# Kernel optimization log

Measured on AMD Instinct MI355X. Metric: run time of the kernel, lower is better.

The kernel has to match this reference:

```python
import jax, jax.numpy as jnp
import numpy as np

B, C, W, H = 16, 256, 32, 32
HEADS = 4


def setup_inputs() -> dict:
    key = jax.random.key(0)
    ks = jax.random.split(key, 9)
    d = C // HEADS
    return {
        "x": jax.random.normal(ks[0], (B, C, W, H), jnp.float32),
        "Wq": jax.random.normal(ks[1], (C, C), jnp.float32) * 0.05,
        "bq": jax.random.normal(ks[2], (C,), jnp.float32) * 0.05,
        "Wk": jax.random.normal(ks[3], (C, C), jnp.float32) * 0.05,
        "bk": jax.random.normal(ks[4], (C,), jnp.float32) * 0.05,
        "Wv": jax.random.normal(ks[5], (C, C), jnp.float32) * 0.05,
        "bv": jax.random.normal(ks[6], (C,), jnp.float32) * 0.05,
        "rel_h": jax.random.normal(ks[7], (1, HEADS, d, 1, H), jnp.float32),
        "rel_w": jax.random.normal(ks[8], (1, HEADS, d, W, 1), jnp.float32),
    }


def reference(x, Wq, bq, Wk, bk, Wv, bv, rel_h, rel_w):
    b, c, w, h = x.shape
    heads = rel_h.shape[1]
    d = c // heads
    n = w * h  # sequence length = spatial positions
    xf = x.reshape(b, c, n)

    def proj(Wt, bt):
        # 1x1 conv == per-position linear over channels
        y = jnp.einsum('oc,bcn->bon', Wt, xf) + bt[None, :, None]
        return y.reshape(b, heads, d, n)

    q = proj(Wq, bq)
    k = proj(Wk, bk)
    v = proj(Wv, bv)

    # similarity = q^T k : [b, heads, n, n]
    sim = jnp.einsum('bhdi,bhdj->bhij', q, k)
    # relative position bias content term: rel^T q
    rel = (rel_h + rel_w).reshape(heads, d, n)  # broadcast-add then flatten spatial
    qpos = jnp.einsum('hdi,bhdj->bhij', rel, q)

    attn = jax.nn.softmax(sim + qpos, axis=-1)
    # out = v @ attn^T : [b, heads, d, n]
    out = jnp.einsum('bhdn,bhmn->bhdm', v, attn)
    return out.reshape(b, c, w, h)
```

## Files before the change

kernel.cpp:

```cpp
#include <hip/hip_runtime.h>

constexpr int Bb  = 16;
constexpr int Cch = 256;
constexpr int NH  = 4;
constexpr int Dh  = 64;
constexpr int Nn  = 1024;

typedef _Float16 f16;
typedef __attribute__((ext_vector_type(8))) _Float16 f16x8;
typedef __attribute__((ext_vector_type(4))) _Float16 f16x4;
typedef __attribute__((ext_vector_type(4))) float    f32x4;

#define LOG2E 1.44269504088896f

__device__ inline void gld16(const f16* g, const f16* lds_wave_base) {
    __builtin_amdgcn_global_load_lds(
        (const __attribute__((address_space(1))) unsigned int*)g,
        (__attribute__((address_space(3))) unsigned int*)lds_wave_base,
        16, 0, 0);
}

__global__ __launch_bounds__(256) void prep_kernel(
    const float* __restrict__ x,
    const float* __restrict__ Wq, const float* __restrict__ Wk,
    const float* __restrict__ Wv,
    const float* __restrict__ rel_h, const float* __restrict__ rel_w,
    f16* __restrict__ xt, f16* __restrict__ Wh, f16* __restrict__ rel_t)
{
    const int gx = blockIdx.x;
    const int t  = threadIdx.x;
    __shared__ float T[64][65];

    if (gx < 1024) {
        const int n0 = (gx & 15) * 64;
        const int c0 = ((gx >> 4) & 3) * 64;
        const int b  = gx >> 6;
        #pragma unroll
        for (int rep = 0; rep < 16; rep++) {
            const int e  = t + rep * 256;
            const int r  = e >> 6;
            const int cc = e & 63;
            T[r][cc] = x[((size_t)b * Cch + c0 + r) * Nn + n0 + cc];
        }
        __syncthreads();
        #pragma unroll
        for (int rep = 0; rep < 4; rep++) {
            const int e  = t + rep * 256;
            const int nn = e >> 4;
            const int c4 = e & 15;
            f16x4 w;
            w.x = (f16)T[c4 * 4 + 0][nn];
            w.y = (f16)T[c4 * 4 + 1][nn];
            w.z = (f16)T[c4 * 4 + 2][nn];
            w.w = (f16)T[c4 * 4 + 3][nn];
            *(f16x4*)&xt[((size_t)b * Nn + n0 + nn) * Cch + c0 + c4 * 4] = w;
        }
    } else if (gx < 2048) {
        const int idx = (gx - 1024) * 256 + t;
        const int d = idx & 63;
        const int n = (idx >> 6) & (Nn - 1);
        const int h = idx >> 16;
        const int hd = h * 64 + d;
        rel_t[idx] = (f16)((rel_h[hd * 32 + (n & 31)] + rel_w[hd * 32 + (n >> 5)])
                           * LOG2E);
    } else {
        const int idx = (gx - 2048) * 256 + t;
        const int og  = idx >> 8;
        const int c   = idx & 255;
        const int p   = og >> 8;
        const int o   = og & 255;
        const float* W = (p == 0) ? Wq : (p == 1) ? Wk : Wv;
        Wh[idx] = (f16)W[o * 256 + c];
    }
}

__global__ __launch_bounds__(256, 3) void gemm_qkv(
    const f16* __restrict__ Wh, const f16* __restrict__ xt,
    const float* __restrict__ bq, const float* __restrict__ bk,
    const float* __restrict__ bv,
    f16* __restrict__ qt, f16* __restrict__ kt, f16* __restrict__ vb)
{
    const int bx   = blockIdx.x;
    const int y    = blockIdx.y;
    const int b    = blockIdx.z;
    const int p    = y >> 1;
    const int half = y & 1;

    __shared__ f16 Wt[128 * 64];
    __shared__ f16 Xt[128 * 64];

    const int t    = threadIdx.x;
    const int wave = t >> 6;
    const int lane = t & 63;
    const int l16  = lane & 15;
    const int quad = lane >> 4;
    const int wm   = wave >> 1;
    const int wsd  = wave & 1;

    f32x4 acc[4][4];
    #pragma unroll
    for (int mi = 0; mi < 4; mi++)
        #pragma unroll
        for (int ni = 0; ni < 4; ni++) acc[mi][ni] = (f32x4){0.f, 0.f, 0.f, 0.f};

    const f16* Wg = Wh + (size_t)y * 128 * 256;
    const f16* Xg = xt + ((size_t)b * Nn + bx * 128) * 256;

    for (int c0 = 0; c0 < 256; c0 += 64) {
        __syncthreads();
        #pragma unroll
        for (int rep = 0; rep < 4; rep++) {
            const int e   = t + rep * 256;
            const int row = e >> 3;
            const int c8s = (e & 7) ^ (row & 7);
            gld16(&Wg[(size_t)row * 256 + c0 + c8s * 8],
                  &Wt[((size_t)rep * 256 + wave * 64) * 8]);
        }
        #pragma unroll
        for (int rep = 0; rep < 4; rep++) {
            const int e   = t + rep * 256;
            const int row = e >> 3;
            const int c8s = (e & 7) ^ (row & 7);
            gld16(&Xg[(size_t)row * 256 + c0 + c8s * 8],
                  &Xt[((size_t)rep * 256 + wave * 64) * 8]);
        }
        __syncthreads();

        const f16* tf = (p < 2) ? Wt : Xt;
        const f16* ts = (p < 2) ? Xt : Wt;
        #pragma unroll
        for (int kk = 0; kk < 2; kk++) {
            f16x8 af[4], bf[4];
            #pragma unroll
            for (int mi = 0; mi < 4; mi++) {
                const int row = wm * 64 + mi * 16 + l16;
                af[mi] = *(const f16x8*)
                    &tf[row * 64 + (((kk * 4 + quad) ^ (row & 7)) << 3)];
            }
            #pragma unroll
            for (int ni = 0; ni < 4; ni++) {
                const int row = wsd * 64 + ni * 16 + l16;
                bf[ni] = *(const f16x8*)
                    &ts[row * 64 + (((kk * 4 + quad) ^ (row & 7)) << 3)];
            }
            #pragma unroll
            for (int mi = 0; mi < 4; mi++)
                #pragma unroll
                for (int ni = 0; ni < 4; ni++)
                    acc[mi][ni] = __builtin_amdgcn_mfma_f32_16x16x32_f16(
                        af[mi], bf[ni], acc[mi][ni], 0, 0, 0);
        }
    }

    const float scale = (p == 1) ? LOG2E : 1.0f;
    if (p < 2) {
        f16* yt = (p == 0) ? qt : kt;
        const float* bg = (p == 0) ? bq : bk;
        #pragma unroll
        for (int mi = 0; mi < 4; mi++) {
            const int o_in = half * 128 + wm * 64 + mi * 16 + quad * 4;
            const float4 b4 = *(const float4*)&bg[o_in];
            const int h = o_in >> 6;
            const int d = o_in & 63;
            #pragma unroll
            for (int ni = 0; ni < 4; ni++) {
                const int n = bx * 128 + wsd * 64 + ni * 16 + l16;
                f16x4 w;
                w.x = (f16)((acc[mi][ni][0] + b4.x) * scale);
                w.y = (f16)((acc[mi][ni][1] + b4.y) * scale);
                w.z = (f16)((acc[mi][ni][2] + b4.z) * scale);
                w.w = (f16)((acc[mi][ni][3] + b4.w) * scale);
                *(f16x4*)&yt[(((size_t)b * NH + h) * Nn + n) * Dh + d] = w;
            }
        }
    } else {
        #pragma unroll
        for (int ni = 0; ni < 4; ni++) {
            const int c  = half * 128 + wsd * 64 + ni * 16 + l16;
            const float bs = bv[c];
            #pragma unroll
            for (int mi = 0; mi < 4; mi++) {
                const int n = bx * 128 + wm * 64 + mi * 16 + quad * 4;
                f16x4 w;
                w.x = (f16)(acc[mi][ni][0] + bs);
                w.y = (f16)(acc[mi][ni][1] + bs);
                w.z = (f16)(acc[mi][ni][2] + bs);
                w.w = (f16)(acc[mi][ni][3] + bs);
                *(f16x4*)&vb[((size_t)b * Cch + c) * Nn + n] = w;
            }
        }
    }
}

__global__ __launch_bounds__(256, 4) void attn_mfma(
    const f16* __restrict__ qt, const f16* __restrict__ kt,
    const f16* __restrict__ relt, const f16* __restrict__ vb,
    float* __restrict__ out)
{
    const int g  = blockIdx.x;
    const int bh = g & 63;
    const int i0 = (g >> 6) * 64;
    const int b  = bh >> 2;
    const int h  = bh & 3;

    const f16* qtb = qt  + (size_t)bh * Nn * Dh;
    const f16* ktb = kt  + (size_t)bh * Nn * Dh;
    const f16* rlt = relt + (size_t)h * Nn * Dh;
    const f16* vbb = vb  + (size_t)(b * Cch + h * Dh) * Nn;

    __shared__ f16 Ka_s[64 * 128];
    __shared__ f16 v_s [64 * 64];
    __shared__ f16 Pt_s[64 * 64];

    const int t    = threadIdx.x;
    const int wave = t >> 6;
    const int lane = t & 63;
    const int l16  = lane & 15;
    const int quad = lane >> 4;

    const int arow = i0 + wave * 16 + l16;
    f16x8 af[4];
    af[0] = *(const f16x8*)&qtb[(size_t)arow * Dh + quad * 8];
    af[1] = *(const f16x8*)&qtb[(size_t)arow * Dh + 32 + quad * 8];
    af[2] = *(const f16x8*)&rlt[(size_t)arow * Dh + quad * 8];
    af[3] = *(const f16x8*)&rlt[(size_t)arow * Dh + 32 + quad * 8];

    f16x8 ones;
    #pragma unroll
    for (int u = 0; u < 8; u++) ones[u] = (f16)1.0f;

    f32x4 Of[4], Ol;
    Ol = (f32x4){0.f, 0.f, 0.f, 0.f};
    #pragma unroll
    for (int ds = 0; ds < 4; ds++) Of[ds] = (f32x4){0.f, 0.f, 0.f, 0.f};
    float m_r[4];
    #pragma unroll
    for (int r = 0; r < 4; r++) m_r[r] = -1e30f;

    for (int j0 = 0; j0 < Nn; j0 += 64) {
        __syncthreads();
        #pragma unroll
        for (int rep = 0; rep < 4; rep++) {
            const int e   = t + rep * 256;
            const int row = e >> 4;
            const int c8s = (e & 15) ^ (row & 7);
            const f16* src = (c8s < 8)
                ? &ktb[(size_t)(j0 + row) * Dh + c8s * 8]
                : &qtb[(size_t)(j0 + row) * Dh + (c8s - 8) * 8];
            gld16(src, &Ka_s[((size_t)rep * 256 + wave * 64) * 8]);
        }
        #pragma unroll
        for (int rep = 0; rep < 2; rep++) {
            const int e   = t + rep * 256;
            const int row = e >> 3;
            const int c8s = (e & 7) ^ (row & 7);
            gld16(&vbb[(size_t)row * Nn + j0 + c8s * 8],
                  &v_s[((size_t)rep * 256 + wave * 64) * 8]);
        }
        __syncthreads();

        f32x4 Sf[4];
        #pragma unroll
        for (int js = 0; js < 4; js++) Sf[js] = (f32x4){0.f, 0.f, 0.f, 0.f};
        #pragma unroll
        for (int k = 0; k < 4; k++) {
            f16x8 bb[4];
            #pragma unroll
            for (int js = 0; js < 4; js++) {
                const int row = js * 16 + l16;
                bb[js] = *(const f16x8*)
                    &Ka_s[row * 128 + (((k * 4 + quad) ^ (row & 7)) << 3)];
            }
            #pragma unroll
            for (int js = 0; js < 4; js++)
                Sf[js] = __builtin_amdgcn_mfma_f32_16x16x32_f16(
                    af[k], bb[js], Sf[js], 0, 0, 0);
        }

        #pragma unroll
        for (int r = 0; r < 4; r++) {
            float tm = fmaxf(fmaxf(Sf[0][r], Sf[1][r]), fmaxf(Sf[2][r], Sf[3][r]));
            tm = fmaxf(tm, __shfl_xor(tm, 1));
            tm = fmaxf(tm, __shfl_xor(tm, 2));
            tm = fmaxf(tm, __shfl_xor(tm, 4));
            tm = fmaxf(tm, __shfl_xor(tm, 8));
            const float mnew  = fmaxf(m_r[r], tm);
            const float alpha = exp2f(m_r[r] - mnew);
            m_r[r] = mnew;

            const int row = wave * 16 + quad * 4 + r;
            const int rx  = row & 7;
            #pragma unroll
            for (int js = 0; js < 4; js++) {
                const float p = exp2f(Sf[js][r] - mnew);
                const int col = js * 16 + l16;
                Pt_s[row * 64 + (((col >> 3) ^ rx) << 3) + (col & 7)] = (f16)p;
            }
            #pragma unroll
            for (int ds = 0; ds < 4; ds++) Of[ds][r] *= alpha;
            Ol[r] *= alpha;
        }

        #pragma unroll
        for (int ks = 0; ks < 2; ks++) {
            const int prow = wave * 16 + l16;
            f16x8 pa = *(const f16x8*)
                &Pt_s[prow * 64 + (((ks * 4 + quad) ^ (prow & 7)) << 3)];
            #pragma unroll
            for (int ds = 0; ds < 4; ds++) {
                const int vrow = ds * 16 + l16;
                f16x8 vv = *(const f16x8*)
                    &v_s[vrow * 64 + (((ks * 4 + quad) ^ (vrow & 7)) << 3)];
                Of[ds] = __builtin_amdgcn_mfma_f32_16x16x32_f16(
                    pa, vv, Of[ds], 0, 0, 0);
            }
            Ol = __builtin_amdgcn_mfma_f32_16x16x32_f16(pa, ones, Ol, 0, 0, 0);
        }
    }

    #pragma unroll
    for (int r = 0; r < 4; r++) {
        const float inv = 1.0f / Ol[r];
        const int i = i0 + wave * 16 + quad * 4 + r;
        #pragma unroll
        for (int ds = 0; ds < 4; ds++) {
            const int d = ds * 16 + l16;
            out[((size_t)(b * Cch + h * Dh + d)) * Nn + i] = Of[ds][r] * inv;
        }
    }
}

extern "C" void kernel_launch(void* const* d_in, const int* in_sizes, int n_in,
                              void* d_out, int out_size, void* d_ws, size_t ws_size,
                              hipStream_t stream)
{
    const float* x     = (const float*)d_in[0];
    const float* Wq    = (const float*)d_in[1];
    const float* bq    = (const float*)d_in[2];
    const float* Wk    = (const float*)d_in[3];
    const float* bk    = (const float*)d_in[4];
    const float* Wv    = (const float*)d_in[5];
    const float* bv    = (const float*)d_in[6];
    const float* rel_h = (const float*)d_in[7];
    const float* rel_w = (const float*)d_in[8];

    f16* ws = (f16*)d_ws;
    const size_t SZQ = (size_t)Bb * NH * Nn * Dh;
    f16* qt   = ws;
    f16* kt   = ws + SZQ;
    f16* vbuf = ws + 2 * SZQ;
    f16* relt = ws + 3 * SZQ;
    f16* xth  = ws + 3 * SZQ + (size_t)NH * Nn * Dh;
    f16* Wh   = xth + SZQ;

    prep_kernel<<<dim3(2816), 256, 0, stream>>>(
        x, Wq, Wk, Wv, rel_h, rel_w, xth, Wh, relt);
    gemm_qkv<<<dim3(Nn / 128, 6, Bb), 256, 0, stream>>>(
        Wh, xth, bq, bk, bv, qt, kt, vbuf);
    attn_mfma<<<dim3(64 * (Nn / 64)), 256, 0, stream>>>(
        qt, kt, relt, vbuf, (float*)d_out);
}
```

Before: 161.4 us.

## Double query rows per attention block to reuse K/V tiles across two subtiles

Each attention block now handles 128 query rows instead of 64, with each wave processing two 16-row subtiles that share the K/Q and V tiles loaded into LDS and the B-fragments read from LDS. This halves the global K/V traffic and the LDS staging per unit of output. In exchange, register pressure roughly doubles (launch bounds lowered to 2 blocks per CU), the grid has half as many blocks (512), and the P scratch buffer grows.

```diff
diff --git a/kernel.cpp b/kernel.cpp
--- a/kernel.cpp
+++ b/kernel.cpp
@@ -192,14 +192,14 @@
     }
 }
 
-__global__ __launch_bounds__(256, 4) void attn_mfma(
+__global__ __launch_bounds__(256, 2) void attn_mfma(
     const f16* __restrict__ qt, const f16* __restrict__ kt,
     const f16* __restrict__ relt, const f16* __restrict__ vb,
     float* __restrict__ out)
 {
     const int g  = blockIdx.x;
     const int bh = g & 63;
-    const int i0 = (g >> 6) * 64;
+    const int i0 = (g >> 6) * 128;
     const int b  = bh >> 2;
     const int h  = bh & 3;
 
@@ -210,7 +210,7 @@
 
     __shared__ f16 Ka_s[64 * 128];
     __shared__ f16 v_s [64 * 64];
-    __shared__ f16 Pt_s[64 * 64];
+    __shared__ f16 Pt_s[128 * 64];
 
     const int t    = threadIdx.x;
     const int wave = t >> 6;
@@ -218,24 +218,30 @@
     const int l16  = lane & 15;
     const int quad = lane >> 4;
 
-    const int arow = i0 + wave * 16 + l16;
-    f16x8 af[4];
-    af[0] = *(const f16x8*)&qtb[(size_t)arow * Dh + quad * 8];
-    af[1] = *(const f16x8*)&qtb[(size_t)arow * Dh + 32 + quad * 8];
-    af[2] = *(const f16x8*)&rlt[(size_t)arow * Dh + quad * 8];
-    af[3] = *(const f16x8*)&rlt[(size_t)arow * Dh + 32 + quad * 8];
+    f16x8 af[2][4];
+    #pragma unroll
+    for (int ms = 0; ms < 2; ms++) {
+        const int arow = i0 + wave * 32 + ms * 16 + l16;
+        af[ms][0] = *(const f16x8*)&qtb[(size_t)arow * Dh + quad * 8];
+        af[ms][1] = *(const f16x8*)&qtb[(size_t)arow * Dh + 32 + quad * 8];
+        af[ms][2] = *(const f16x8*)&rlt[(size_t)arow * Dh + quad * 8];
+        af[ms][3] = *(const f16x8*)&rlt[(size_t)arow * Dh + 32 + quad * 8];
+    }
 
     f16x8 ones;
     #pragma unroll
     for (int u = 0; u < 8; u++) ones[u] = (f16)1.0f;
 
-    f32x4 Of[4], Ol;
-    Ol = (f32x4){0.f, 0.f, 0.f, 0.f};
-    #pragma unroll
-    for (int ds = 0; ds < 4; ds++) Of[ds] = (f32x4){0.f, 0.f, 0.f, 0.f};
-    float m_r[4];
-    #pragma unroll
-    for (int r = 0; r < 4; r++) m_r[r] = -1e30f;
+    f32x4 Of[2][4], Ol[2];
+    float m_r[2][4];
+    #pragma unroll
+    for (int ms = 0; ms < 2; ms++) {
+        Ol[ms] = (f32x4){0.f, 0.f, 0.f, 0.f};
+        #pragma unroll
+        for (int ds = 0; ds < 4; ds++) Of[ms][ds] = (f32x4){0.f, 0.f, 0.f, 0.f};
+        #pragma unroll
+        for (int r = 0; r < 4; r++) m_r[ms][r] = -1e30f;
+    }
 
     for (int j0 = 0; j0 < Nn; j0 += 64) {
         __syncthreads();
@@ -259,9 +265,11 @@
         }
         __syncthreads();
 
-        f32x4 Sf[4];
-        #pragma unroll
-        for (int js = 0; js < 4; js++) Sf[js] = (f32x4){0.f, 0.f, 0.f, 0.f};
+        f32x4 Sf[2][4];
+        #pragma unroll
+        for (int ms = 0; ms < 2; ms++)
+            #pragma unroll
+            for (int js = 0; js < 4; js++) Sf[ms][js] = (f32x4){0.f, 0.f, 0.f, 0.f};
         #pragma unroll
         for (int k = 0; k < 4; k++) {
             f16x8 bb[4];
@@ -272,60 +280,76 @@
                     &Ka_s[row * 128 + (((k * 4 + quad) ^ (row & 7)) << 3)];
             }
             #pragma unroll
-            for (int js = 0; js < 4; js++)
-                Sf[js] = __builtin_amdgcn_mfma_f32_16x16x32_f16(
-                    af[k], bb[js], Sf[js], 0, 0, 0);
-        }
-
-        #pragma unroll
-        for (int r = 0; r < 4; r++) {
-            float tm = fmaxf(fmaxf(Sf[0][r], Sf[1][r]), fmaxf(Sf[2][r], Sf[3][r]));
-            tm = fmaxf(tm, __shfl_xor(tm, 1));
-            tm = fmaxf(tm, __shfl_xor(tm, 2));
-            tm = fmaxf(tm, __shfl_xor(tm, 4));
-            tm = fmaxf(tm, __shfl_xor(tm, 8));
-            const float mnew  = fmaxf(m_r[r], tm);
-            const float alpha = exp2f(m_r[r] - mnew);
-            m_r[r] = mnew;
-
-            const int row = wave * 16 + quad * 4 + r;
-            const int rx  = row & 7;
-            #pragma unroll
-            for (int js = 0; js < 4; js++) {
-                const float p = exp2f(Sf[js][r] - mnew);
-                const int col = js * 16 + l16;
-                Pt_s[row * 64 + (((col >> 3) ^ rx) << 3) + (col & 7)] = (f16)p;
-            }
-            #pragma unroll
-            for (int ds = 0; ds < 4; ds++) Of[ds][r] *= alpha;
-            Ol[r] *= alpha;
+            for (int ms = 0; ms < 2; ms++)
+                #pragma unroll
+                for (int js = 0; js < 4; js++)
+                    Sf[ms][js] = __builtin_amdgcn_mfma_f32_16x16x32_f16(
+                        af[ms][k], bb[js], Sf[ms][js], 0, 0, 0);
+        }
+
+        #pragma unroll
+        for (int ms = 0; ms < 2; ms++) {
+            #pragma unroll
+            for (int r = 0; r < 4; r++) {
+                float tm = fmaxf(fmaxf(Sf[ms][0][r], Sf[ms][1][r]),
+                                 fmaxf(Sf[ms][2][r], Sf[ms][3][r]));
+                tm = fmaxf(tm, __shfl_xor(tm, 1));
+                tm = fmaxf(tm, __shfl_xor(tm, 2));
+                tm = fmaxf(tm, __shfl_xor(tm, 4));
+                tm = fmaxf(tm, __shfl_xor(tm, 8));
+                const float mnew  = fmaxf(m_r[ms][r], tm);
+                const float alpha = exp2f(m_r[ms][r] - mnew);
+                m_r[ms][r] = mnew;
+
+                const int row = wave * 32 + ms * 16 + quad * 4 + r;
+                const int rx  = row & 7;
+                #pragma unroll
+                for (int js = 0; js < 4; js++) {
+                    const float p = exp2f(Sf[ms][js][r] - mnew);
+                    const int col = js * 16 + l16;
+                    Pt_s[row * 64 + (((col >> 3) ^ rx) << 3) + (col & 7)] = (f16)p;
+                }
+                #pragma unroll
+                for (int ds = 0; ds < 4; ds++) Of[ms][ds][r] *= alpha;
+                Ol[ms][r] *= alpha;
+            }
         }
 
         #pragma unroll
         for (int ks = 0; ks < 2; ks++) {
-            const int prow = wave * 16 + l16;
-            f16x8 pa = *(const f16x8*)
-                &Pt_s[prow * 64 + (((ks * 4 + quad) ^ (prow & 7)) << 3)];
+            f16x8 vv[4];
             #pragma unroll
             for (int ds = 0; ds < 4; ds++) {
                 const int vrow = ds * 16 + l16;
-                f16x8 vv = *(const f16x8*)
+                vv[ds] = *(const f16x8*)
                     &v_s[vrow * 64 + (((ks * 4 + quad) ^ (vrow & 7)) << 3)];
-                Of[ds] = __builtin_amdgcn_mfma_f32_16x16x32_f16(
-                    pa, vv, Of[ds], 0, 0, 0);
-            }
-            Ol = __builtin_amdgcn_mfma_f32_16x16x32_f16(pa, ones, Ol, 0, 0, 0);
-        }
-    }
-
-    #pragma unroll
-    for (int r = 0; r < 4; r++) {
-        const float inv = 1.0f / Ol[r];
-        const int i = i0 + wave * 16 + quad * 4 + r;
-        #pragma unroll
-        for (int ds = 0; ds < 4; ds++) {
-            const int d = ds * 16 + l16;
-            out[((size_t)(b * Cch + h * Dh + d)) * Nn + i] = Of[ds][r] * inv;
+            }
+            #pragma unroll
+            for (int ms = 0; ms < 2; ms++) {
+                const int prow = wave * 32 + ms * 16 + l16;
+                f16x8 pa = *(const f16x8*)
+                    &Pt_s[prow * 64 + (((ks * 4 + quad) ^ (prow & 7)) << 3)];
+                #pragma unroll
+                for (int ds = 0; ds < 4; ds++)
+                    Of[ms][ds] = __builtin_amdgcn_mfma_f32_16x16x32_f16(
+                        pa, vv[ds], Of[ms][ds], 0, 0, 0);
+                Ol[ms] = __builtin_amdgcn_mfma_f32_16x16x32_f16(
+                    pa, ones, Ol[ms], 0, 0, 0);
+            }
+        }
+    }
+
+    #pragma unroll
+    for (int ms = 0; ms < 2; ms++) {
+        #pragma unroll
+        for (int r = 0; r < 4; r++) {
+            const float inv = 1.0f / Ol[ms][r];
+            const int i = i0 + wave * 32 + ms * 16 + quad * 4 + r;
+            #pragma unroll
+            for (int ds = 0; ds < 4; ds++) {
+                const int d = ds * 16 + l16;
+                out[((size_t)(b * Cch + h * Dh + d)) * Nn + i] = Of[ms][ds][r] * inv;
+            }
         }
     }
 }
@@ -357,6 +381,6 @@
         x, Wq, Wk, Wv, rel_h, rel_w, xth, Wh, relt);
     gemm_qkv<<<dim3(Nn / 128, 6, Bb), 256, 0, stream>>>(
         Wh, xth, bq, bk, bv, qt, kt, vbuf);
-    attn_mfma<<<dim3(64 * (Nn / 64)), 256, 0, stream>>>(
+    attn_mfma<<<dim3(64 * (Nn / 128)), 256, 0, stream>>>(
         qt, kt, relt, vbuf, (float*)d_out);
 }
```

After: 160.5 us. Within noise of the previous version (-0.5%).
